# Kernel tuning notes

Hardware: AMD Instinct MI355X
Metric: run time of the kernel (lower is better)

The kernel has to match this reference:

```python
import math
import jax, jax.numpy as jnp
import numpy as np

DIM = 1024
FFN_DIM = 4096
NUM_HEADS = 16
HEAD_DIM = DIM // NUM_HEADS
SCALE = 1.0 / math.sqrt(HEAD_DIM)
EPS = 1e-5


def _layer_norm(x, gamma, beta):
    mu = jnp.mean(x, axis=-1, keepdims=True)
    var = jnp.mean(jnp.square(x - mu), axis=-1, keepdims=True)
    return (x - mu) * jax.lax.rsqrt(var + EPS) * gamma + beta


def _gelu_erf(x):
    # matches torch GELU module: x * 0.5 * (1 + erf(x / sqrt(2)))
    return x * 0.5 * (1.0 + jax.lax.erf(x / math.sqrt(2.0)))


def setup_inputs() -> dict:
    key = jax.random.key(0)
    ks = jax.random.split(key, 12)
    B, L = 2, 2048
    s = 0.02
    inp = {
        "x": jax.random.normal(ks[0], (B, L, DIM), dtype=jnp.float32),
        "g1": jnp.ones((DIM,), jnp.float32),
        "b1": jnp.zeros((DIM,), jnp.float32),
        "Wq": jax.random.normal(ks[1], (DIM, DIM), jnp.float32) * s,
        "bq": jnp.zeros((DIM,), jnp.float32),
        "Wk": jax.random.normal(ks[2], (DIM, DIM), jnp.float32) * s,
        "bk": jnp.zeros((DIM,), jnp.float32),
        "Wv": jax.random.normal(ks[3], (DIM, DIM), jnp.float32) * s,
        "bv": jnp.zeros((DIM,), jnp.float32),
        "Wo": jax.random.normal(ks[4], (DIM, DIM), jnp.float32) * s,
        "bo": jnp.zeros((DIM,), jnp.float32),
        "g2": jnp.ones((DIM,), jnp.float32),
        "b2": jnp.zeros((DIM,), jnp.float32),
        "W1": jax.random.normal(ks[5], (FFN_DIM, DIM), jnp.float32) * s,
        "bf1": jnp.zeros((FFN_DIM,), jnp.float32),
        "W2": jax.random.normal(ks[6], (DIM, FFN_DIM), jnp.float32) * s,
        "bf2": jnp.zeros((DIM,), jnp.float32),
    }
    return inp


def reference(x, g1, b1, Wq, bq, Wk, bk, Wv, bv, Wo, bo, g2, b2, W1, bf1, W2, bf2):
    B, L, C = x.shape
    n, c = NUM_HEADS, HEAD_DIM

    # ---- pre-norm self-attention ----
    h = _layer_norm(x, g1, b1)
    q = (h @ Wq.T + bq).reshape(B, L, n, c)
    k = (h @ Wk.T + bk).reshape(B, L, n, c)
    v = (h @ Wv.T + bv).reshape(B, L, n, c)
    attn = SCALE * jnp.einsum('binc,bjnc->bnij', q, k)   # [B, n, L, L]
    attn = jax.nn.softmax(attn, axis=-1)
    o = jnp.einsum('bnij,bjnc->binc', attn, v).reshape(B, L, C)
    x = x + (o @ Wo.T + bo)

    # ---- pre-norm FFN (GELU, erf form) ----
    h = _layer_norm(x, g2, b2)
    h = _gelu_erf(h @ W1.T + bf1)
    x = x + (h @ W2.T + bf2)
    return x
```

## Files before the change

kernel.cpp:

```cpp
#include <hip/hip_runtime.h>
#include <hip/hip_bf16.h>
#include <math.h>

typedef unsigned short u16;
typedef __attribute__((ext_vector_type(8))) __bf16 bf16x8;
typedef __attribute__((ext_vector_type(4))) float f32x4;

#define DIM   1024
#define LSEQ  2048
#define BTOK  4096
#define HD    64
#define FFN   4096
#define QSCL  0.18033688011112042f

__device__ __forceinline__ u16 f2bf(float f) {
  unsigned u = __builtin_bit_cast(unsigned, f);
  u += 0x7FFFu + ((u >> 16) & 1u);
  return (u16)(u >> 16);
}
__device__ __forceinline__ unsigned pk2(float a, float b) {
  return (unsigned)f2bf(a) | ((unsigned)f2bf(b) << 16);
}
__device__ __forceinline__ unsigned cvtpk(float lo, float hi) {
  unsigned r;
  asm("v_cvt_pk_bf16_f32 %0, %1, %2" : "=v"(r) : "v"(lo), "v"(hi));
  return r;
}
__device__ __forceinline__ f32x4 mfma16(bf16x8 a, bf16x8 b, f32x4 c) {
  return __builtin_amdgcn_mfma_f32_16x16x32_bf16(a, b, c, 0, 0, 0);
}
__device__ __forceinline__ void gload16(const void* g, void* l) {
  __builtin_amdgcn_global_load_lds((const __attribute__((address_space(1))) char*)g,
                                   (__attribute__((address_space(3))) char*)l, 16, 0, 0);
}
__device__ __forceinline__ float gelu_t(float v) {
  float v3 = v * v * v;
  float tt = fmaf(-0.10296766f, v3, -2.30258509f * v);
  return v * __builtin_amdgcn_rcpf(1.0f + exp2f(tt));
}

__global__ __launch_bounds__(256) void ln_kernel(const float* __restrict__ x,
                                                 const float* __restrict__ g,
                                                 const float* __restrict__ bta,
                                                 u16* __restrict__ out) {
  int row = blockIdx.x, t = threadIdx.x;
  const float* xr = x + (size_t)row * DIM;
  float4 xv = *(const float4*)(xr + t * 4);
  float s  = xv.x + xv.y + xv.z + xv.w;
  float ss = xv.x * xv.x + xv.y * xv.y + xv.z * xv.z + xv.w * xv.w;
#pragma unroll
  for (int m = 32; m >= 1; m >>= 1) {
    s  += __shfl_xor(s, m);
    ss += __shfl_xor(ss, m);
  }
  __shared__ float red[8];
  if ((t & 63) == 0) { red[(t >> 6) * 2] = s; red[(t >> 6) * 2 + 1] = ss; }
  __syncthreads();
  s  = red[0] + red[2] + red[4] + red[6];
  ss = red[1] + red[3] + red[5] + red[7];
  float mu  = s * (1.0f / DIM);
  float var = ss * (1.0f / DIM) - mu * mu;
  float rs  = rsqrtf(var + 1e-5f);
  float4 gv = *(const float4*)(g + t * 4);
  float4 bv = *(const float4*)(bta + t * 4);
  uint2 o;
  o.x = pk2((xv.x - mu) * rs * gv.x + bv.x, (xv.y - mu) * rs * gv.y + bv.y);
  o.y = pk2((xv.z - mu) * rs * gv.z + bv.z, (xv.w - mu) * rs * gv.w + bv.w);
  *(uint2*)(out + (size_t)row * DIM + t * 4) = o;
}

__global__ __launch_bounds__(256) void wcvt4(const float* __restrict__ Wq, const float* __restrict__ Wk,
                                             const float* __restrict__ Wv, const float* __restrict__ Wo,
                                             u16* __restrict__ dst) {
  int b = blockIdx.x;
  int r = b >> 9;
  const float* s = (r == 0) ? Wq : (r == 1) ? Wk : (r == 2) ? Wv : Wo;
  size_t i = (((size_t)(b & 511)) * 256 + threadIdx.x) * 8;
  float4 f0 = *(const float4*)(s + i), f1 = *(const float4*)(s + i + 4);
  uint4 o = { pk2(f0.x, f0.y), pk2(f0.z, f0.w), pk2(f1.x, f1.y), pk2(f1.z, f1.w) };
  *(uint4*)(dst + ((size_t)r << 20) + i) = o;
}
__global__ __launch_bounds__(256) void wcvt2(const float* __restrict__ W1, const float* __restrict__ W2,
                                             u16* __restrict__ d1, u16* __restrict__ d2) {
  int b = blockIdx.x;
  const float* s = (b < 2048) ? W1 : W2;
  u16* d = (b < 2048) ? d1 : d2;
  size_t i = (((size_t)(b & 2047)) * 256 + threadIdx.x) * 8;
  float4 f0 = *(const float4*)(s + i), f1 = *(const float4*)(s + i + 4);
  uint4 o = { pk2(f0.x, f0.y), pk2(f0.z, f0.w), pk2(f1.x, f1.y), pk2(f1.z, f1.w) };
  *(uint4*)(d + i) = o;
}

__global__ __launch_bounds__(256) void transpose_v(const u16* __restrict__ v,
                                                   u16* __restrict__ vt) {
  __shared__ u16 tls[64][80];
  int jb = blockIdx.x, bh = blockIdx.y, b = bh >> 4, h = bh & 15;
  int t = threadIdx.x;
  int r = t >> 2, seg = t & 3;
  const u16* src = v + (size_t)(b * LSEQ + jb * 64 + r) * DIM + h * HD + seg * 16;
  *(uint4*)&tls[r][seg * 16]     = *(const uint4*)src;
  *(uint4*)&tls[r][seg * 16 + 8] = *(const uint4*)(src + 8);
  __syncthreads();
  int c = t >> 2, jseg = t & 3;
  u16 tmp[16] __attribute__((aligned(16)));
#pragma unroll
  for (int i = 0; i < 16; i++) tmp[i] = tls[jseg * 16 + i][c];
  u16* dst = vt + ((size_t)bh * HD + c) * LSEQ + jb * 64 + jseg * 16;
  *(uint4*)dst       = *(const uint4*)tmp;
  *(uint4*)(dst + 8) = *(const uint4*)(tmp + 8);
}

struct GArg { const u16* Wb; const float* bias; u16* outB; float oscale; };

template <int EPI, int BM>
__global__ __launch_bounds__(256) void gemm3(const u16* __restrict__ A,
                                             GArg g0, GArg g1, GArg g2,
                                             const float* __restrict__ resid,
                                             float* __restrict__ outF,
                                             int N, int K, int nbPerW) {
  constexpr int WM = BM / 32;
  __shared__ u16 lsa[2][BM * 32];
  __shared__ u16 lsb[2][128 * 32];
  const int t = threadIdx.x;
  const int w = t >> 6, l = t & 63, l15 = l & 15, lg = l >> 4;
  const int wr = w >> 1, wc = w & 1;
  const int nwg = gridDim.x * gridDim.y;
  int flat = blockIdx.y * gridDim.x + blockIdx.x;
  flat = (flat & 7) * (nwg >> 3) + (flat >> 3);
  const int bx = flat % gridDim.x, by = flat / gridDim.x;
  const int sel = bx / nbPerW, nb = bx % nbPerW;
  GArg G = (sel == 0) ? g0 : ((sel == 1) ? g1 : g2);
  const int n0 = nb * 128, m0 = by * BM;

  f32x4 acc[WM][4];
#pragma unroll
  for (int m = 0; m < WM; m++)
#pragma unroll
    for (int n = 0; n < 4; n++) acc[m][n] = (f32x4){0.f, 0.f, 0.f, 0.f};

  const int grow = t >> 2;
  const int gcol = 8 * ((t & 3) ^ ((t >> 3) & 3));
  const u16* Asrc = A + (size_t)(m0 + grow) * K + gcol;
  const u16* Bsrc = G.Wb + (size_t)(n0 + grow) * K + gcol;
  const int rs = (l15 >> 1) & 3;

  auto stage = [&](int k0, int buf) {
#pragma unroll
    for (int i = 0; i < BM / 64; i++)
      gload16(Asrc + (size_t)i * 64 * K + k0, (char*)lsa + buf * (BM * 64) + i * 4096 + w * 1024);
#pragma unroll
    for (int i = 0; i < 2; i++)
      gload16(Bsrc + (size_t)i * 64 * K + k0, (char*)lsb + buf * 8192 + i * 4096 + w * 1024);
  };

  stage(0, 0);
  const int NT = K >> 5;
  for (int it = 0; it < NT; it++) {
    const int buf = it & 1;
    __syncthreads();
    if (it + 1 < NT) stage((it + 1) << 5, buf ^ 1);

    bf16x8 af[WM], bfr[4];
#pragma unroll
    for (int m = 0; m < WM; m++)
      af[m] = *(const bf16x8*)&lsa[buf][(wr * (BM / 2) + m * 16 + l15) * 32 + (lg ^ rs) * 8];
#pragma unroll
    for (int n = 0; n < 4; n++)
      bfr[n] = *(const bf16x8*)&lsb[buf][(wc * 64 + n * 16 + l15) * 32 + (lg ^ rs) * 8];
#pragma unroll
    for (int m = 0; m < WM; m++)
#pragma unroll
      for (int n = 0; n < 4; n++)
        acc[m][n] = mfma16(af[m], bfr[n], acc[m][n]);
  }

#pragma unroll
  for (int m = 0; m < WM; m++) {
    const int row = m0 + wr * (BM / 2) + m * 16 + lg * 4;
#pragma unroll
    for (int n = 0; n < 4; n++) {
      const int col = n0 + wc * 64 + n * 16 + l15;
      const float bias = G.bias[col];
#pragma unroll
      for (int r = 0; r < 4; r++) {
        const float v = acc[m][n][r] + bias;
        const size_t idx = (size_t)(row + r) * N + col;
        if (EPI == 0)      G.outB[idx] = f2bf(v * G.oscale);
        else if (EPI == 1) outF[idx] = v + resid[idx];
        else               G.outB[idx] = f2bf(gelu_t(v));
      }
    }
  }
}

__global__ __launch_bounds__(256) void attn4(const u16* __restrict__ q,
                                             const u16* __restrict__ k,
                                             const u16* __restrict__ vt,
                                             u16* __restrict__ o) {
  __shared__ u16 kls[2][64 * 64];
  __shared__ u16 vls[2][64 * 64];
  __shared__ u16 pls[4][16 * 64];
  const int t = threadIdx.x, w = t >> 6, l = t & 63, l15 = l & 15, lg = l >> 4;
  const int qbk = blockIdx.x, bh = blockIdx.y, b = bh >> 4, h = bh & 15;
  const int qrow0 = b * LSEQ + qbk * 64 + w * 16;

  bf16x8 av[2];
#pragma unroll
  for (int i = 0; i < 2; i++)
    av[i] = *(const bf16x8*)(q + (size_t)(qrow0 + l15) * DIM + h * HD + i * 32 + lg * 8);

  const int grow = t >> 3, gchk = t & 7;
  const u16* ksrc = k + (size_t)(b * LSEQ + grow) * DIM + h * HD + 8 * (gchk ^ (grow & 7));
  const u16* vsrc = vt + ((size_t)bh * HD + grow) * LSEQ + 8 * (gchk ^ (grow & 7));

  f32x4 oacc[4];
#pragma unroll
  for (int cb = 0; cb < 4; cb++) oacc[cb] = (f32x4){0.f, 0.f, 0.f, 0.f};
  float mrun = -INFINITY;
  float lsum = 0.f;
  u16* pw = &pls[w][0];

  auto issueTile = [&](int jt, int buf) {
    const u16* kp = ksrc + (size_t)jt * DIM;
    const u16* vp = vsrc + jt;
#pragma unroll
    for (int i = 0; i < 2; i++) {
      gload16(kp + (size_t)i * 32 * DIM,  (char*)&kls[buf][0] + i * 4096 + w * 1024);
      gload16(vp + (size_t)i * 32 * LSEQ, (char*)&vls[buf][0] + i * 4096 + w * 1024);
    }
  };

  issueTile(0, 0);
  for (int it = 0; it < LSEQ / 64; it++) {
    const int buf = it & 1;
    __syncthreads();
    if (it + 1 < LSEQ / 64) issueTile((it + 1) * 64, buf ^ 1);

    f32x4 s[4];
#pragma unroll
    for (int cb = 0; cb < 4; cb++) s[cb] = (f32x4){0.f, 0.f, 0.f, 0.f};
    const u16* kb = &kls[buf][0];
    __builtin_amdgcn_s_setprio(1);
#pragma unroll
    for (int i = 0; i < 2; i++) {
#pragma unroll
      for (int cb = 0; cb < 4; cb++) {
        const int krow = cb * 16 + l15;
        bf16x8 kf = *(const bf16x8*)&kb[krow * 64 + (((i << 2) | lg) ^ (krow & 7)) * 8];
        s[cb] = mfma16(kf, av[i], s[cb]);
      }
    }
    __builtin_amdgcn_s_setprio(0);

    float tm = fmaxf(fmaxf(fmaxf(s[0][0], s[0][1]), fmaxf(s[0][2], s[0][3])),
                     fmaxf(fmaxf(fmaxf(s[1][0], s[1][1]), fmaxf(s[1][2], s[1][3])),
                           fmaxf(fmaxf(fmaxf(s[2][0], s[2][1]), fmaxf(s[2][2], s[2][3])),
                                 fmaxf(fmaxf(s[3][0], s[3][1]), fmaxf(s[3][2], s[3][3])))));
    if (__any(tm > mrun + 8.0f)) {
      float tr = fmaxf(tm, __shfl_xor(tm, 16));
      tr = fmaxf(tr, __shfl_xor(tr, 32));
      const float mn = fmaxf(mrun, tr);
      const float scl = exp2f(mrun - mn);
      mrun = mn;
      lsum *= scl;
#pragma unroll
      for (int r = 0; r < 4; r++) {
        const float so = __shfl(scl, lg * 4 + r);
#pragma unroll
        for (int cb = 0; cb < 4; cb++) oacc[cb][r] *= so;
      }
    }
    float ps = 0.f;
    uint2 pk[4];
#pragma unroll
    for (int cb = 0; cb < 4; cb++) {
      float a0 = exp2f(s[cb][0] - mrun);
      float a1 = exp2f(s[cb][1] - mrun);
      float a2 = exp2f(s[cb][2] - mrun);
      float a3 = exp2f(s[cb][3] - mrun);
      ps += (a0 + a1) + (a2 + a3);
      pk[cb].x = cvtpk(a0, a1);
      pk[cb].y = cvtpk(a2, a3);
    }
    lsum += ps;
#pragma unroll
    for (int cb = 0; cb < 4; cb++) {
      const int c = 2 * cb + (lg >> 1);
      *(uint2*)((char*)pw + l15 * 128 + ((c ^ (l15 & 7)) * 16) + (lg & 1) * 8) = pk[cb];
    }

    const u16* vb = &vls[buf][0];
#pragma unroll
    for (int kt = 0; kt < 2; kt++) {
      bf16x8 pa = *(const bf16x8*)((char*)pw + l15 * 128 + (((4 * kt + lg) ^ (l15 & 7)) * 16));
      __builtin_amdgcn_s_setprio(1);
#pragma unroll
      for (int cb = 0; cb < 4; cb++) {
        const int vrow = cb * 16 + l15;
        bf16x8 vf = *(const bf16x8*)&vb[vrow * 64 + (((kt << 2) | lg) ^ (vrow & 7)) * 8];
        oacc[cb] = mfma16(pa, vf, oacc[cb]);
      }
      __builtin_amdgcn_s_setprio(0);
    }
  }

  float rl = lsum + __shfl_xor(lsum, 16);
  rl += __shfl_xor(rl, 32);
#pragma unroll
  for (int r = 0; r < 4; r++) {
    const float lo = __shfl(rl, lg * 4 + r);
    const float rcp = 1.0f / lo;
#pragma unroll
    for (int cb = 0; cb < 4; cb++) {
      o[(size_t)(qrow0 + lg * 4 + r) * DIM + h * HD + cb * 16 + l15] =
          f2bf(oacc[cb][r] * rcp);
    }
  }
}

extern "C" void kernel_launch(void* const* d_in, const int* in_sizes, int n_in,
                              void* d_out, int out_size, void* d_ws, size_t ws_size,
                              hipStream_t stream) {
  const float* x   = (const float*)d_in[0];
  const float* g1  = (const float*)d_in[1];
  const float* b1  = (const float*)d_in[2];
  const float* Wq  = (const float*)d_in[3];
  const float* bq  = (const float*)d_in[4];
  const float* Wk  = (const float*)d_in[5];
  const float* bk  = (const float*)d_in[6];
  const float* Wv  = (const float*)d_in[7];
  const float* bv  = (const float*)d_in[8];
  const float* Wo  = (const float*)d_in[9];
  const float* bo  = (const float*)d_in[10];
  const float* g2  = (const float*)d_in[11];
  const float* b2  = (const float*)d_in[12];
  const float* W1  = (const float*)d_in[13];
  const float* bf1 = (const float*)d_in[14];
  const float* W2  = (const float*)d_in[15];
  const float* bf2 = (const float*)d_in[16];
  float* out = (float*)d_out;

  const size_t E = (size_t)BTOK * DIM;
  u16* h     = (u16*)d_ws;
  u16* qb    = h + E;
  u16* kbuf  = qb + E;
  u16* vbuf  = kbuf + E;
  u16* vtb   = vbuf + E;
  u16* wqkvo = vtb + E;
  u16* ob    = vbuf;
  u16* W1b   = qb;
  u16* W2b   = kbuf;
  u16* mid   = vbuf;
  u16* h2    = h;
  float* x2  = out;

  u16* Wqb = wqkvo;
  u16* Wkb = wqkvo + ((size_t)1 << 20);
  u16* Wvb = wqkvo + ((size_t)2 << 20);
  u16* Wob = wqkvo + ((size_t)3 << 20);

  wcvt4<<<dim3(2048), dim3(256), 0, stream>>>(Wq, Wk, Wv, Wo, wqkvo);
  ln_kernel<<<dim3(BTOK), dim3(256), 0, stream>>>(x, g1, b1, h);
  gemm3<0, 128><<<dim3(24, BTOK / 128), 256, 0, stream>>>(
      h, GArg{Wqb, bq, qb, QSCL}, GArg{Wkb, bk, kbuf, 1.0f}, GArg{Wvb, bv, vbuf, 1.0f},
      nullptr, nullptr, DIM, DIM, 8);
  transpose_v<<<dim3(32, 32), 256, 0, stream>>>(vbuf, vtb);
  attn4<<<dim3(LSEQ / 64, 32), 256, 0, stream>>>(qb, kbuf, vtb, ob);
  {
    GArg s{Wob, bo, nullptr, 1.0f};
    gemm3<1, 64><<<dim3(8, BTOK / 64), 256, 0, stream>>>(ob, s, s, s, x, x2, DIM, DIM, 8);
  }
  wcvt2<<<dim3(4096), dim3(256), 0, stream>>>(W1, W2, W1b, W2b);
  ln_kernel<<<dim3(BTOK), dim3(256), 0, stream>>>(x2, g2, b2, h2);
  {
    GArg s{W1b, bf1, mid, 1.0f};
    gemm3<2, 128><<<dim3(32, BTOK / 128), 256, 0, stream>>>(h2, s, s, s, nullptr, nullptr, FFN, DIM, 32);
  }
  {
    GArg s{W2b, bf2, nullptr, 1.0f};
    gemm3<1, 64><<<dim3(8, BTOK / 64), 256, 0, stream>>>(mid, s, s, s, x2, out, DIM, FFN, 8);
  }
}
```

Measured before the change: 278.0 us.

## Fold running max into MFMA accumulator init and precompute LDS addresses in attention

The attention kernel now subtracts the running max by seeding the QK^T MFMA accumulator with the negated max, so the per-element subtraction before exp2 disappears. It also switches exp2f to the raw hardware builtin and precomputes swizzled LDS addresses in both attention and GEMM. It also remaps the attention grid so blocks sharing a head land on the same XCD, and adds an occupancy hint to the launch bounds. The intent is to cut VALU work in the softmax and address arithmetic in inner loops, and to improve L2 reuse of K/V. The risk is subtle numerical differences from the raw exp2 and from the rescale threshold now being relative to an offset accumulator.

```diff
diff --git a/kernel.cpp b/kernel.cpp
--- a/kernel.cpp
+++ b/kernel.cpp
@@ -13,6 +13,12 @@
 #define FFN   4096
 #define QSCL  0.18033688011112042f
 
+#if __has_builtin(__builtin_amdgcn_exp2f)
+#define EXP2(x) __builtin_amdgcn_exp2f(x)
+#else
+#define EXP2(x) exp2f(x)
+#endif
+
 __device__ __forceinline__ u16 f2bf(float f) {
   unsigned u = __builtin_bit_cast(unsigned, f);
   u += 0x7FFFu + ((u >> 16) & 1u);
@@ -36,7 +42,7 @@
 __device__ __forceinline__ float gelu_t(float v) {
   float v3 = v * v * v;
   float tt = fmaf(-0.10296766f, v3, -2.30258509f * v);
-  return v * __builtin_amdgcn_rcpf(1.0f + exp2f(tt));
+  return v * __builtin_amdgcn_rcpf(1.0f + EXP2(tt));
 }
 
 __global__ __launch_bounds__(256) void ln_kernel(const float* __restrict__ x,
@@ -119,6 +125,7 @@
                                              float* __restrict__ outF,
                                              int N, int K, int nbPerW) {
   constexpr int WM = BM / 32;
+  constexpr int ABUF = BM * 64;
   __shared__ u16 lsa[2][BM * 32];
   __shared__ u16 lsb[2][128 * 32];
   const int t = threadIdx.x;
@@ -144,10 +151,13 @@
   const u16* Bsrc = G.Wb + (size_t)(n0 + grow) * K + gcol;
   const int rs = (l15 >> 1) & 3;
 
+  const char* aadr = (const char*)lsa + (wr * (BM / 2) + l15) * 64 + (lg ^ rs) * 16;
+  const char* badr = (const char*)lsb + (wc * 64 + l15) * 64 + (lg ^ rs) * 16;
+
   auto stage = [&](int k0, int buf) {
 #pragma unroll
     for (int i = 0; i < BM / 64; i++)
-      gload16(Asrc + (size_t)i * 64 * K + k0, (char*)lsa + buf * (BM * 64) + i * 4096 + w * 1024);
+      gload16(Asrc + (size_t)i * 64 * K + k0, (char*)lsa + buf * ABUF + i * 4096 + w * 1024);
 #pragma unroll
     for (int i = 0; i < 2; i++)
       gload16(Bsrc + (size_t)i * 64 * K + k0, (char*)lsb + buf * 8192 + i * 4096 + w * 1024);
@@ -160,13 +170,15 @@
     __syncthreads();
     if (it + 1 < NT) stage((it + 1) << 5, buf ^ 1);
 
+    const char* ap = aadr + buf * ABUF;
+    const char* bp = badr + buf * 8192;
     bf16x8 af[WM], bfr[4];
 #pragma unroll
     for (int m = 0; m < WM; m++)
-      af[m] = *(const bf16x8*)&lsa[buf][(wr * (BM / 2) + m * 16 + l15) * 32 + (lg ^ rs) * 8];
+      af[m] = *(const bf16x8*)(ap + m * 1024);
 #pragma unroll
     for (int n = 0; n < 4; n++)
-      bfr[n] = *(const bf16x8*)&lsb[buf][(wc * 64 + n * 16 + l15) * 32 + (lg ^ rs) * 8];
+      bfr[n] = *(const bf16x8*)(bp + n * 1024);
 #pragma unroll
     for (int m = 0; m < WM; m++)
 #pragma unroll
@@ -193,21 +205,34 @@
   }
 }
 
-__global__ __launch_bounds__(256) void attn4(const u16* __restrict__ q,
-                                             const u16* __restrict__ k,
-                                             const u16* __restrict__ vt,
-                                             u16* __restrict__ o) {
-  __shared__ u16 kls[2][64 * 64];
-  __shared__ u16 vls[2][64 * 64];
-  __shared__ u16 pls[4][16 * 64];
+__global__ __launch_bounds__(256, 4) void attn5(const u16* __restrict__ q,
+                                                const u16* __restrict__ k,
+                                                const u16* __restrict__ vt,
+                                                u16* __restrict__ o) {
+  __shared__ __align__(16) char smem[40960];
   const int t = threadIdx.x, w = t >> 6, l = t & 63, l15 = l & 15, lg = l >> 4;
-  const int qbk = blockIdx.x, bh = blockIdx.y, b = bh >> 4, h = bh & 15;
+  int flat = blockIdx.y * gridDim.x + blockIdx.x;
+  flat = (flat & 7) * 128 + (flat >> 3);
+  const int qbk = flat & 31, bh = flat >> 5;
+  const int b = bh >> 4, h = bh & 15;
   const int qrow0 = b * LSEQ + qbk * 64 + w * 16;
+  const int r7 = l15 & 7;
+  const int c0 = lg ^ r7;
 
   bf16x8 av[2];
 #pragma unroll
   for (int i = 0; i < 2; i++)
     av[i] = *(const bf16x8*)(q + (size_t)(qrow0 + l15) * DIM + h * HD + i * 32 + lg * 8);
+
+  const char* adrA  = smem + l15 * 128 + c0 * 16;
+  const char* adrB  = smem + l15 * 128 + (c0 ^ 4) * 16;
+  const char* padrA = smem + 32768 + w * 2048 + l15 * 128 + c0 * 16;
+  const char* padrB = smem + 32768 + w * 2048 + l15 * 128 + (c0 ^ 4) * 16;
+  char* pwa[4];
+#pragma unroll
+  for (int cb = 0; cb < 4; cb++)
+    pwa[cb] = smem + 32768 + w * 2048 + l15 * 128 +
+              (((2 * cb + (lg >> 1)) ^ r7) * 16) + (lg & 1) * 8;
 
   const int grow = t >> 3, gchk = t & 7;
   const u16* ksrc = k + (size_t)(b * LSEQ + grow) * DIM + h * HD + 8 * (gchk ^ (grow & 7));
@@ -216,17 +241,16 @@
   f32x4 oacc[4];
 #pragma unroll
   for (int cb = 0; cb < 4; cb++) oacc[cb] = (f32x4){0.f, 0.f, 0.f, 0.f};
-  float mrun = -INFINITY;
+  f32x4 minit = (f32x4){0.f, 0.f, 0.f, 0.f};
   float lsum = 0.f;
-  u16* pw = &pls[w][0];
 
   auto issueTile = [&](int jt, int buf) {
     const u16* kp = ksrc + (size_t)jt * DIM;
     const u16* vp = vsrc + jt;
 #pragma unroll
     for (int i = 0; i < 2; i++) {
-      gload16(kp + (size_t)i * 32 * DIM,  (char*)&kls[buf][0] + i * 4096 + w * 1024);
-      gload16(vp + (size_t)i * 32 * LSEQ, (char*)&vls[buf][0] + i * 4096 + w * 1024);
+      gload16(kp + (size_t)i * 32 * DIM,  smem + buf * 8192 + i * 4096 + w * 1024);
+      gload16(vp + (size_t)i * 32 * LSEQ, smem + 16384 + buf * 8192 + i * 4096 + w * 1024);
     }
   };
 
@@ -235,20 +259,18 @@
     const int buf = it & 1;
     __syncthreads();
     if (it + 1 < LSEQ / 64) issueTile((it + 1) * 64, buf ^ 1);
+    const int ko = buf * 8192;
 
     f32x4 s[4];
-#pragma unroll
-    for (int cb = 0; cb < 4; cb++) s[cb] = (f32x4){0.f, 0.f, 0.f, 0.f};
-    const u16* kb = &kls[buf][0];
+    const char* kA = adrA + ko;
+    const char* kB = adrB + ko;
     __builtin_amdgcn_s_setprio(1);
 #pragma unroll
-    for (int i = 0; i < 2; i++) {
-#pragma unroll
-      for (int cb = 0; cb < 4; cb++) {
-        const int krow = cb * 16 + l15;
-        bf16x8 kf = *(const bf16x8*)&kb[krow * 64 + (((i << 2) | lg) ^ (krow & 7)) * 8];
-        s[cb] = mfma16(kf, av[i], s[cb]);
-      }
+    for (int cb = 0; cb < 4; cb++) {
+      bf16x8 kf0 = *(const bf16x8*)(kA + cb * 2048);
+      bf16x8 kf1 = *(const bf16x8*)(kB + cb * 2048);
+      s[cb] = mfma16(kf0, av[0], minit);
+      s[cb] = mfma16(kf1, av[1], s[cb]);
     }
     __builtin_amdgcn_s_setprio(0);
 
@@ -256,13 +278,16 @@
                      fmaxf(fmaxf(fmaxf(s[1][0], s[1][1]), fmaxf(s[1][2], s[1][3])),
                            fmaxf(fmaxf(fmaxf(s[2][0], s[2][1]), fmaxf(s[2][2], s[2][3])),
                                  fmaxf(fmaxf(s[3][0], s[3][1]), fmaxf(s[3][2], s[3][3])))));
-    if (__any(tm > mrun + 8.0f)) {
+    if (__any(tm > 8.0f)) {
       float tr = fmaxf(tm, __shfl_xor(tm, 16));
       tr = fmaxf(tr, __shfl_xor(tr, 32));
-      const float mn = fmaxf(mrun, tr);
-      const float scl = exp2f(mrun - mn);
-      mrun = mn;
+      const float d = fmaxf(tr, 0.f);
+      const float scl = EXP2(-d);
+      const f32x4 dv = (f32x4){d, d, d, d};
       lsum *= scl;
+      minit -= dv;
+#pragma unroll
+      for (int cb = 0; cb < 4; cb++) s[cb] -= dv;
 #pragma unroll
       for (int r = 0; r < 4; r++) {
         const float so = __shfl(scl, lg * 4 + r);
@@ -274,34 +299,34 @@
     uint2 pk[4];
 #pragma unroll
     for (int cb = 0; cb < 4; cb++) {
-      float a0 = exp2f(s[cb][0] - mrun);
-      float a1 = exp2f(s[cb][1] - mrun);
-      float a2 = exp2f(s[cb][2] - mrun);
-      float a3 = exp2f(s[cb][3] - mrun);
+      float a0 = EXP2(s[cb][0]);
+      float a1 = EXP2(s[cb][1]);
+      float a2 = EXP2(s[cb][2]);
+      float a3 = EXP2(s[cb][3]);
       ps += (a0 + a1) + (a2 + a3);
       pk[cb].x = cvtpk(a0, a1);
       pk[cb].y = cvtpk(a2, a3);
     }
     lsum += ps;
 #pragma unroll
+    for (int cb = 0; cb < 4; cb++) *(uint2*)pwa[cb] = pk[cb];
+
+    const char* vA = adrA + ko + 16384;
+    const char* vB = adrB + ko + 16384;
+    bf16x8 pa0 = *(const bf16x8*)padrA;
+    bf16x8 pa1 = *(const bf16x8*)padrB;
+    __builtin_amdgcn_s_setprio(1);
+#pragma unroll
     for (int cb = 0; cb < 4; cb++) {
-      const int c = 2 * cb + (lg >> 1);
-      *(uint2*)((char*)pw + l15 * 128 + ((c ^ (l15 & 7)) * 16) + (lg & 1) * 8) = pk[cb];
-    }
-
-    const u16* vb = &vls[buf][0];
-#pragma unroll
-    for (int kt = 0; kt < 2; kt++) {
-      bf16x8 pa = *(const bf16x8*)((char*)pw + l15 * 128 + (((4 * kt + lg) ^ (l15 & 7)) * 16));
-      __builtin_amdgcn_s_setprio(1);
-#pragma unroll
-      for (int cb = 0; cb < 4; cb++) {
-        const int vrow = cb * 16 + l15;
-        bf16x8 vf = *(const bf16x8*)&vb[vrow * 64 + (((kt << 2) | lg) ^ (vrow & 7)) * 8];
-        oacc[cb] = mfma16(pa, vf, oacc[cb]);
-      }
-      __builtin_amdgcn_s_setprio(0);
-    }
+      bf16x8 vf0 = *(const bf16x8*)(vA + cb * 2048);
+      oacc[cb] = mfma16(pa0, vf0, oacc[cb]);
+    }
+#pragma unroll
+    for (int cb = 0; cb < 4; cb++) {
+      bf16x8 vf1 = *(const bf16x8*)(vB + cb * 2048);
+      oacc[cb] = mfma16(pa1, vf1, oacc[cb]);
+    }
+    __builtin_amdgcn_s_setprio(0);
   }
 
   float rl = lsum + __shfl_xor(lsum, 16);
@@ -365,7 +390,7 @@
       h, GArg{Wqb, bq, qb, QSCL}, GArg{Wkb, bk, kbuf, 1.0f}, GArg{Wvb, bv, vbuf, 1.0f},
       nullptr, nullptr, DIM, DIM, 8);
   transpose_v<<<dim3(32, 32), 256, 0, stream>>>(vbuf, vtb);
-  attn4<<<dim3(LSEQ / 64, 32), 256, 0, stream>>>(qb, kbuf, vtb, ob);
+  attn5<<<dim3(LSEQ / 64, 32), 256, 0, stream>>>(qb, kbuf, vtb, ob);
   {
     GArg s{Wob, bo, nullptr, 1.0f};
     gemm3<1, 64><<<dim3(8, BTOK / 64), 256, 0, stream>>>(ob, s, s, s, x, x2, DIM, DIM, 8);
```

After: 255.0 us. 1.09x faster.
